# Performance work log

Hardware: AMD Instinct MI355X
Metric: run time of the kernel (lower is better)

Reference implementation:

```python
import jax, jax.numpy as jnp
import numpy as np

N = 50000      # num nodes
E = 800000     # num edges
F = 128        # num_node_features
H = 4          # num_heads
D = 32         # output_dim (per head); H*D == F -> residual is identity
G = 8          # grid_size
K = 3          # spline order (standard KANLinear default)
NEG_SLOPE = 0.2


def _make_grid(grid_size, k):
    # uniform grid on [-1, 1], extended by k on each side: [G + 2k + 1] points
    h = 2.0 / grid_size
    return jnp.arange(-k, grid_size + k + 1, dtype=jnp.float32) * h - 1.0


def _bsplines(x, grid, k):
    # x: [N, F], grid: [G+2k+1] -> bases: [N, F, G+k] (Cox-de Boor recursion)
    xg = x[..., None]
    b = ((xg >= grid[:-1]) & (xg < grid[1:])).astype(x.dtype)
    for j in range(1, k + 1):
        left = (xg - grid[:-(j + 1)]) / (grid[j:-1] - grid[:-(j + 1)]) * b[..., :-1]
        right = (grid[j + 1:] - xg) / (grid[j + 1:] - grid[1:-j]) * b[..., 1:]
        b = left + right
    return b


def _kan_linear(x, base_w, spline_w, grid, k):
    # efficient-KAN linear, no bias: silu(x) @ Wb^T + Bspline(x) contracted with Ws
    base = jax.nn.silu(x) @ base_w.T                      # [N, O]
    bs = _bsplines(x, grid, k)                            # [N, F, G+K]
    spline = jnp.einsum('nfc,ofc->no', bs, spline_w)      # [N, O]
    return base + spline


def setup_inputs() -> dict:
    key = jax.random.key(0)
    ks = jax.random.split(key, 8)
    O = H * D
    C = G + K
    x = jax.random.normal(ks[0], (N, F), dtype=jnp.float32)
    edge_index = jax.random.randint(ks[1], (2, E), 0, N, dtype=jnp.int64)
    scale = 1.0 / np.sqrt(F)
    base_w_src = jax.random.normal(ks[2], (O, F), dtype=jnp.float32) * scale
    spline_w_src = jax.random.normal(ks[3], (O, F, C), dtype=jnp.float32) * (0.1 * scale)
    base_w_dst = jax.random.normal(ks[4], (O, F), dtype=jnp.float32) * scale
    spline_w_dst = jax.random.normal(ks[5], (O, F, C), dtype=jnp.float32) * (0.1 * scale)
    double_attn = jax.random.normal(ks[6], (1, H, D), dtype=jnp.float32) * (1.0 / np.sqrt(D))
    bias = jnp.zeros((O,), dtype=jnp.float32)
    prelu_a = jnp.asarray(0.25, dtype=jnp.float32)  # nn.PReLU default
    return {"x": x, "edge_index": edge_index,
            "base_w_src": base_w_src, "spline_w_src": spline_w_src,
            "base_w_dst": base_w_dst, "spline_w_dst": spline_w_dst,
            "double_attn": double_attn, "bias": bias, "prelu_a": prelu_a}


def reference(x, edge_index, base_w_src, spline_w_src, base_w_dst, spline_w_dst,
              double_attn, bias, prelu_a):
    grid = _make_grid(G, K)
    src = edge_index[0]
    dst = edge_index[1]
    num_nodes = x.shape[0]
    # projections (dropout is identity in eval mode)
    sp = _kan_linear(x, base_w_src, spline_w_src, grid, K).reshape(num_nodes, H, D)
    dp = _kan_linear(x, base_w_dst, spline_w_dst, grid, K).reshape(num_nodes, H, D)
    # GATv2 edge scores: leakyrelu(gather(src) + gather(dst)), then attn vector dot
    e = jax.nn.leaky_relu(sp[src] + dp[dst], NEG_SLOPE)          # [E, H, D]
    attn = jnp.sum(double_attn * e, axis=-1)                     # [E, H]
    # segment softmax over incoming edges per destination node (global max shift, as in torch)
    exp_attn = jnp.exp(attn - jnp.max(attn))                     # [E, H]
    denom = jax.ops.segment_sum(exp_attn, dst, num_segments=num_nodes)  # [Nn, H]
    alpha = exp_attn / (denom[dst] + 1e-16)                      # [E, H]
    # weighted aggregation
    msg = sp[src] * alpha[..., None]                             # [E, H, D]
    out = jax.ops.segment_sum(msg, dst, num_segments=num_nodes)  # [Nn, H, D]
    # residual: num_node_features == H*D -> identity
    out = out + x.reshape(num_nodes, H, D)
    # concat heads + bias + PReLU activation
    out = out.reshape(num_nodes, H * D) + bias
    return jnp.where(out >= 0, out, prelu_a * out)
```

## Files before the change

kernel.cpp:

```cpp
#include <hip/hip_runtime.h>
#include <math.h>

#define NN 50000
#define EE 800000
#define FF 128
#define CC 11
#define O2 256
#define KT 1536
#define NKC 8
#define AROW 200
#define NPB 768
#define NTB2 224
#define NFB 1563
#define NPACK 424
#define NTN 896
#define CAP 64

typedef __attribute__((ext_vector_type(8))) short short8;
typedef __attribute__((ext_vector_type(4))) float f32x4;
typedef unsigned int uint;
typedef unsigned short ushort;

__device__ __forceinline__ ushort bf16_rne(float v) {
  uint u = __float_as_uint(v);
  u = u + 0x7FFFu + ((u >> 16) & 1u);
  return (ushort)(u >> 16);
}
__device__ __forceinline__ float bf_lo(uint u) { return __uint_as_float(u << 16); }
__device__ __forceinline__ float bf_hi(uint u) { return __uint_as_float(u & 0xffff0000u); }

__device__ __forceinline__ void lds_barrier() {
  asm volatile("s_waitcnt lgkmcnt(0)" ::: "memory");
  __builtin_amdgcn_s_barrier();
}

__global__ __launch_bounds__(256) void repack_zero_kernel(
    const float* __restrict__ bws, const float* __restrict__ sws,
    const float* __restrict__ bwd, const float* __restrict__ swd,
    ushort* __restrict__ Wh, int* __restrict__ cur) {
  int idx = blockIdx.x * 256 + threadIdx.x;
  if (idx < NN) cur[idx] = 0;
  if (idx >= O2 * KT) return;
  int j = idx & 7;
  int lane = (idx >> 3) & 63;
  int cg = (idx >> 9) & 15;
  int g = idx >> 13;
  int col = cg * 16 + (lane & 15);
  int k = g * 32 + (lane >> 4) * 8 + j;
  int f = k / 12;
  int ch = k - f * 12;
  const float* bw = (col < 128) ? bws : bwd;
  const float* sw = (col < 128) ? sws : swd;
  int o = col & 127;
  float v = (ch == 11) ? bw[(size_t)o * FF + f] : sw[((size_t)o * FF + f) * CC + ch];
  Wh[idx] = bf16_rne(v);
}

__device__ __forceinline__ void kan_row(float xv, ushort* row) {
  row[11] = bf16_rne(xv / (1.f + __expf(-xv)));
  float u = fmaf(xv, 4.f, 7.f);
  float fj = floorf(u);
  int j = (int)fj;
  if (j >= 0 && j <= 13) {
    float tt = u - fj;
    float t2 = tt * tt, t3 = t2 * tt;
    float w0 = (1.f / 6.f) * (1.f - 3.f * tt + 3.f * t2 - t3);
    float w1 = (1.f / 6.f) * (4.f - 6.f * t2 + 3.f * t3);
    float w2 = (1.f / 6.f) * (1.f + 3.f * tt + 3.f * t2 - 3.f * t3);
    float w3 = (1.f / 6.f) * t3;
    float wv[4] = {w0, w1, w2, w3};
    int i0 = j - 3;
#pragma unroll
    for (int c = 0; c < 4; ++c) {
      int idx = i0 + c;
      if (idx >= 0 && idx <= 10) row[idx] = bf16_rne(wv[c]);
    }
  }
}

__global__ __launch_bounds__(256) void proj_tail_kernel(
    const float* __restrict__ x, const ushort* __restrict__ Wh,
    uint* __restrict__ projB, float2* __restrict__ projF) {
  __shared__ ushort Ah[2][64][AROW];
  const int t = threadIdx.x;
  const int lane = t & 63;
  const int w = t >> 6;
  const int m = lane & 15;
  const int quad = lane >> 4;

  if (blockIdx.x >= NPB) {
    ushort(*Ath)[AROW] = Ah[0];
    const int tb = blockIdx.x - NPB;
    const int ks = tb & 7;
    const int rest = tb >> 3;
    const int tg = rest >> 1;
    const int hh = rest & 1;
    const int block0 = NPB * 64 + tg * 64;
    const int gn = block0 + lane;
    const bool valid = (gn < NN);

    {
      const float4 zero4 = make_float4(0.f, 0.f, 0.f, 0.f);
      float4 xvv = valid ? *(const float4*)(x + (size_t)gn * FF + ks * 16 + w * 4) : zero4;
      float xa[4] = {xvv.x, xvv.y, xvv.z, xvv.w};
      uint4* dz = (uint4*)&Ath[lane][w * 48];
#pragma unroll
      for (int i = 0; i < 6; ++i) dz[i] = make_uint4(0u, 0u, 0u, 0u);
#pragma unroll
      for (int jf = 0; jf < 4; ++jf) kan_row(xa[jf], &Ath[lane][w * 48 + jf * 12]);
    }

    f32x4 acc[4][2];
#pragma unroll
    for (int r = 0; r < 4; ++r)
#pragma unroll
      for (int c = 0; c < 2; ++c) acc[r][c] = (f32x4)(0.f);

    short8 bh_c[2];
#pragma unroll
    for (int c = 0; c < 2; ++c)
      bh_c[c] = *(const short8*)(Wh + (size_t)((ks * 6) * 16 + hh * 8 + w * 2 + c) * 512 +
                                 (size_t)lane * 8);
    __syncthreads();

#pragma unroll
    for (int sk = 0; sk < 6; ++sk) {
      short8 bh_n[2];
      if (sk < 5) {
#pragma unroll
        for (int c = 0; c < 2; ++c)
          bh_n[c] = *(const short8*)(Wh +
                                     (size_t)((ks * 6 + sk + 1) * 16 + hh * 8 + w * 2 + c) * 512 +
                                     (size_t)lane * 8);
      }
      short8 a0 = *(const short8*)(&Ath[0 * 16 + m][sk * 32 + quad * 8]);
      short8 a1 = *(const short8*)(&Ath[1 * 16 + m][sk * 32 + quad * 8]);
      short8 a2 = *(const short8*)(&Ath[2 * 16 + m][sk * 32 + quad * 8]);
      short8 a3 = *(const short8*)(&Ath[3 * 16 + m][sk * 32 + quad * 8]);
#pragma unroll
      for (int c = 0; c < 2; ++c) {
        acc[0][c] = __builtin_amdgcn_mfma_f32_16x16x32_bf16(a0, bh_c[c], acc[0][c], 0, 0, 0);
        acc[1][c] = __builtin_amdgcn_mfma_f32_16x16x32_bf16(a1, bh_c[c], acc[1][c], 0, 0, 0);
        acc[2][c] = __builtin_amdgcn_mfma_f32_16x16x32_bf16(a2, bh_c[c], acc[2][c], 0, 0, 0);
        acc[3][c] = __builtin_amdgcn_mfma_f32_16x16x32_bf16(a3, bh_c[c], acc[3][c], 0, 0, 0);
      }
      bh_c[0] = bh_n[0];
      bh_c[1] = bh_n[1];
    }
    const int q = hh * 4 + w;
#pragma unroll
    for (int r = 0; r < 4; ++r) {
#pragma unroll
      for (int reg = 0; reg < 4; ++reg) {
        int nl = r * 16 + quad * 4 + reg;
        projF[(size_t)(ks * NTN + tg * 64 + nl) * 128 + q * 16 + m] =
            make_float2(acc[r][0][reg], acc[r][1][reg]);
      }
    }
    return;
  }

  const int block0 = blockIdx.x * 64;
  const int gn = block0 + lane;

  auto stage = [&](float4 xvv, ushort(*buf)[AROW]) {
    float xa[4] = {xvv.x, xvv.y, xvv.z, xvv.w};
    uint4* dz = (uint4*)&buf[lane][w * 48];
#pragma unroll
    for (int i = 0; i < 6; ++i) dz[i] = make_uint4(0u, 0u, 0u, 0u);
#pragma unroll
    for (int jf = 0; jf < 4; ++jf) kan_row(xa[jf], &buf[lane][w * 48 + jf * 12]);
  };

  f32x4 acc[4][4];
#pragma unroll
  for (int r = 0; r < 4; ++r)
#pragma unroll
    for (int c = 0; c < 4; ++c) acc[r][c] = (f32x4)(0.f);

  float4 xv0 = *(const float4*)(x + (size_t)gn * FF + w * 4);
  stage(xv0, Ah[0]);
  float4 xv_next = *(const float4*)(x + (size_t)gn * FF + 16 + w * 4);

  short8 bh[2][4];
#pragma unroll
  for (int c = 0; c < 4; ++c) {
    bh[0][c] = *(const short8*)(Wh + (size_t)(0 * 16 + w * 4 + c) * 512 + (size_t)lane * 8);
    bh[1][c] = *(const short8*)(Wh + (size_t)(1 * 16 + w * 4 + c) * 512 + (size_t)lane * 8);
  }
  lds_barrier();

#pragma unroll 2
  for (int kc = 0; kc < NKC; ++kc) {
    float4 xv_pf = make_float4(0.f, 0.f, 0.f, 0.f);
    if (kc + 2 < NKC)
      xv_pf = *(const float4*)(x + (size_t)gn * FF + (kc + 2) * 16 + w * 4);
    if (kc + 1 < NKC) stage(xv_next, Ah[(kc + 1) & 1]);
#pragma unroll
    for (int sk = 0; sk < 6; ++sk) {
      const int p = sk & 1;
      short8 a0 = *(const short8*)(&Ah[kc & 1][0 * 16 + m][sk * 32 + quad * 8]);
      short8 a1 = *(const short8*)(&Ah[kc & 1][1 * 16 + m][sk * 32 + quad * 8]);
#pragma unroll
      for (int c = 0; c < 4; ++c)
        acc[0][c] = __builtin_amdgcn_mfma_f32_16x16x32_bf16(a0, bh[p][c], acc[0][c], 0, 0, 0);
#pragma unroll
      for (int c = 0; c < 4; ++c)
        acc[1][c] = __builtin_amdgcn_mfma_f32_16x16x32_bf16(a1, bh[p][c], acc[1][c], 0, 0, 0);
      short8 a2 = *(const short8*)(&Ah[kc & 1][2 * 16 + m][sk * 32 + quad * 8]);
      short8 a3 = *(const short8*)(&Ah[kc & 1][3 * 16 + m][sk * 32 + quad * 8]);
#pragma unroll
      for (int c = 0; c < 4; ++c)
        acc[2][c] = __builtin_amdgcn_mfma_f32_16x16x32_bf16(a2, bh[p][c], acc[2][c], 0, 0, 0);
#pragma unroll
      for (int c = 0; c < 4; ++c)
        acc[3][c] = __builtin_amdgcn_mfma_f32_16x16x32_bf16(a3, bh[p][c], acc[3][c], 0, 0, 0);
      int gnc = kc * 6 + sk + 2;
      if (gnc > 47) gnc = 47;
#pragma unroll
      for (int c = 0; c < 4; ++c)
        bh[p][c] = *(const short8*)(Wh + (size_t)(gnc * 16 + w * 4 + c) * 512 +
                                    (size_t)lane * 8);
    }
    lds_barrier();
    xv_next = xv_pf;
  }
#pragma unroll
  for (int r = 0; r < 4; ++r) {
#pragma unroll
    for (int reg = 0; reg < 4; ++reg) {
      int nd = block0 + r * 16 + quad * 4 + reg;
#pragma unroll
      for (int cp = 0; cp < 2; ++cp) {
        int q = 2 * w + cp;
        uint val = (uint)bf16_rne(acc[r][2 * cp][reg]) |
                   ((uint)bf16_rne(acc[r][2 * cp + 1][reg]) << 16);
        projB[(size_t)nd * 128 + q * 16 + m] = val;
      }
    }
  }
}

__global__ __launch_bounds__(256) void fill_kernel(
    const int* __restrict__ ei, int* __restrict__ cur, ushort* __restrict__ scsr) {
  int base = (blockIdx.x * 256 + threadIdx.x) * 2;
  if (base + 1 < EE) {
    int2 ss = *(const int2*)(ei + base);
    int2 dd = *(const int2*)(ei + EE + base);
    int p0 = atomicAdd(&cur[dd.x], 1);
    if (p0 < CAP) scsr[(size_t)dd.x * CAP + p0] = (ushort)ss.x;
    int p1 = atomicAdd(&cur[dd.y], 1);
    if (p1 < CAP) scsr[(size_t)dd.y * CAP + p1] = (ushort)ss.y;
  } else if (base < EE) {
    int s = ei[base], d = ei[EE + base];
    int p0 = atomicAdd(&cur[d], 1);
    if (p0 < CAP) scsr[(size_t)d * CAP + p0] = (ushort)s;
  }
}

__global__ __launch_bounds__(256) void pack_kernel(
    const float2* __restrict__ projF, uint* __restrict__ projB) {
  int wk = blockIdx.x * 256 + threadIdx.x;
  int n = wk >> 7, p = wk & 127;
  if (n < 848) {
    float lo = 0.f, hi = 0.f;
#pragma unroll
    for (int ks = 0; ks < 8; ++ks) {
      float2 v = projF[(size_t)(ks * NTN + n) * 128 + p];
      lo += v.x;
      hi += v.y;
    }
    projB[(size_t)(NPB * 64 + n) * 128 + p] =
        (uint)bf16_rne(lo) | ((uint)bf16_rne(hi) << 16);
  }
}

__global__ __launch_bounds__(256) void aggr_kernel(
    const uint* __restrict__ projB, const ushort* __restrict__ scsr,
    const int* __restrict__ cur, const float* __restrict__ av,
    const float* __restrict__ x, const float* __restrict__ bias,
    const float* __restrict__ pa, float* __restrict__ out) {
  int d = blockIdx.x * 4 + (threadIdx.x >> 6);
  if (d >= NN) return;
  int l = threadIdx.x & 63;
  int g = l >> 4, m = l & 15;
  const uint4* pb4 = (const uint4*)projB;
  int sv = (int)scsr[(size_t)d * CAP + l];
  uint4 dpu = pb4[(size_t)d * 32 + 16 + m];
  uint du[4] = {dpu.x, dpu.y, dpu.z, dpu.w};
  float dplo[4], dphi[4], avlo[4], avhi[4];
  int cl[4];
#pragma unroll
  for (int j = 0; j < 4; ++j) {
    dplo[j] = bf_lo(du[j]);
    dphi[j] = bf_hi(du[j]);
    int p = 4 * m + j;
    cl[j] = ((p >> 4) << 5) + (p & 15);
    avlo[j] = av[cl[j]];
    avhi[j] = av[cl[j] + 16];
  }
  int cnt = cur[d];
  if (cnt > CAP) cnt = CAP;
  float acl[4] = {0.f, 0.f, 0.f, 0.f}, ach[4] = {0.f, 0.f, 0.f, 0.f};
  float den = 0.f;
  if (cnt > 0 && g < cnt) {
    const int cm = cnt - 1;
    int e1 = g + 4, e2 = g + 8;
    int s0 = __shfl(sv, g, 64);
    int s1 = __shfl(sv, e1 < cm ? e1 : cm, 64);
    int s2 = __shfl(sv, e2 < cm ? e2 : cm, 64);
    uint4 U0 = pb4[(size_t)s0 * 32 + m];
    uint4 U1 = pb4[(size_t)s1 * 32 + m];
    uint4 U2 = pb4[(size_t)s2 * 32 + m];
    for (int e = g; e < cnt; e += 4) {
      int e3 = e + 12;
      int s3 = __shfl(sv, e3 < cm ? e3 : cm, 64);
      uint4 U3 = pb4[(size_t)s3 * 32 + m];
      uint uu[4] = {U0.x, U0.y, U0.z, U0.w};
      float slo[4], shi[4];
      float vp = 0.f;
#pragma unroll
      for (int j = 0; j < 4; ++j) {
        slo[j] = bf_lo(uu[j]);
        shi[j] = bf_hi(uu[j]);
        float v0 = slo[j] + dplo[j];
        float v1 = shi[j] + dphi[j];
        v0 = (v0 >= 0.f) ? v0 : 0.2f * v0;
        v1 = (v1 >= 0.f) ? v1 : 0.2f * v1;
        vp = fmaf(v0, avlo[j], vp);
        vp = fmaf(v1, avhi[j], vp);
      }
      vp += __shfl_xor(vp, 1, 64);
      vp += __shfl_xor(vp, 2, 64);
      float e_ = __expf(vp);
#pragma unroll
      for (int j = 0; j < 4; ++j) {
        acl[j] = fmaf(e_, slo[j], acl[j]);
        ach[j] = fmaf(e_, shi[j], ach[j]);
      }
      den += e_;
      U0 = U1;
      U1 = U2;
      U2 = U3;
    }
  }
#pragma unroll
  for (int off = 16; off < 64; off <<= 1) {
    den += __shfl_xor(den, off, 64);
#pragma unroll
    for (int j = 0; j < 4; ++j) {
      acl[j] += __shfl_xor(acl[j], off, 64);
      ach[j] += __shfl_xor(ach[j], off, 64);
    }
  }
  if (g == 0) {
    float a = pa[0];
    float r = 1.f / (den + 1e-16f);
#pragma unroll
    for (int j = 0; j < 4; ++j) {
      float o0 = acl[j] * r + x[(size_t)d * FF + cl[j]] + bias[cl[j]];
      float o1 = ach[j] * r + x[(size_t)d * FF + cl[j] + 16] + bias[cl[j] + 16];
      out[(size_t)d * FF + cl[j]] = (o0 >= 0.f) ? o0 : a * o0;
      out[(size_t)d * FF + cl[j] + 16] = (o1 >= 0.f) ? o1 : a * o1;
    }
  }
}

extern "C" void kernel_launch(void* const* d_in, const int* in_sizes, int n_in,
                              void* d_out, int out_size, void* d_ws, size_t ws_size,
                              hipStream_t stream) {
  const float* x = (const float*)d_in[0];
  const int* ei = (const int*)d_in[1];
  const float* bws = (const float*)d_in[2];
  const float* sws = (const float*)d_in[3];
  const float* bwd = (const float*)d_in[4];
  const float* swd = (const float*)d_in[5];
  const float* av = (const float*)d_in[6];
  const float* bias = (const float*)d_in[7];
  const float* pa = (const float*)d_in[8];

  ushort* Wh = (ushort*)d_ws;
  uint* projB = (uint*)(Wh + (size_t)O2 * KT);
  int* cur = (int*)(projB + (size_t)NN * 128);
  ushort* scsr = (ushort*)(cur + NN);
  float2* projF = (float2*)(scsr + (size_t)NN * CAP);

  repack_zero_kernel<<<(O2 * KT + 255) / 256, 256, 0, stream>>>(bws, sws, bwd, swd, Wh, cur);
  proj_tail_kernel<<<NPB + NTB2, 256, 0, stream>>>(x, Wh, projB, projF);
  fill_kernel<<<NFB, 256, 0, stream>>>(ei, cur, scsr);
  pack_kernel<<<NPACK, 256, 0, stream>>>(projF, projB);
  aggr_kernel<<<(NN + 3) / 4, 256, 0, stream>>>(projB, scsr, cur, av, x, bias, pa,
                                                (float*)d_out);
}
```

Measured before the change: 221.4 us.

## Privatize CSR fill counters per XCC to avoid cross-die atomic contention

The fill kernel now reads the hardware XCC id and writes each edge into one of eight per-XCC bucket arrays, each with its own counter and a capacity of 24 per destination. This keeps the atomics and scattered stores local to one die instead of contending across dies. The aggregation kernel reads all eight counters, computes prefix offsets, and gathers each lane's source index from the matching bucket. In exchange it zeroes an eight times larger counter array, adds eight counter loads per destination, and truncates edges if one XCC gets more than 24 edges for a node.

```diff
diff --git a/kernel.cpp b/kernel.cpp
--- a/kernel.cpp
+++ b/kernel.cpp
@@ -15,6 +15,7 @@
 #define NPACK 424
 #define NTN 896
 #define CAP 64
+#define CAP8 24
 
 typedef __attribute__((ext_vector_type(8))) short short8;
 typedef __attribute__((ext_vector_type(4))) float f32x4;
@@ -37,9 +38,11 @@
 __global__ __launch_bounds__(256) void repack_zero_kernel(
     const float* __restrict__ bws, const float* __restrict__ sws,
     const float* __restrict__ bwd, const float* __restrict__ swd,
-    ushort* __restrict__ Wh, int* __restrict__ cur) {
+    ushort* __restrict__ Wh, int* __restrict__ cur8) {
   int idx = blockIdx.x * 256 + threadIdx.x;
-  if (idx < NN) cur[idx] = 0;
+  if (idx < 8 * NN) cur8[idx] = 0;
+  int idx2 = idx + 393216;
+  if (idx2 < 8 * NN) cur8[idx2] = 0;
   if (idx >= O2 * KT) return;
   int j = idx & 7;
   int lane = (idx >> 3) & 63;
@@ -242,19 +245,25 @@
 }
 
 __global__ __launch_bounds__(256) void fill_kernel(
-    const int* __restrict__ ei, int* __restrict__ cur, ushort* __restrict__ scsr) {
+    const int* __restrict__ ei, int* __restrict__ cur8, ushort* __restrict__ scsr8) {
+  uint xcc;
+  asm volatile("s_getreg_b32 %0, hwreg(HW_REG_XCC_ID)" : "=s"(xcc));
+  xcc &= 7;
   int base = (blockIdx.x * 256 + threadIdx.x) * 2;
   if (base + 1 < EE) {
     int2 ss = *(const int2*)(ei + base);
     int2 dd = *(const int2*)(ei + EE + base);
-    int p0 = atomicAdd(&cur[dd.x], 1);
-    if (p0 < CAP) scsr[(size_t)dd.x * CAP + p0] = (ushort)ss.x;
-    int p1 = atomicAdd(&cur[dd.y], 1);
-    if (p1 < CAP) scsr[(size_t)dd.y * CAP + p1] = (ushort)ss.y;
+    size_t b0 = (size_t)xcc * NN + dd.x;
+    int p0 = atomicAdd(&cur8[b0], 1);
+    if (p0 < CAP8) scsr8[b0 * CAP8 + p0] = (ushort)ss.x;
+    size_t b1 = (size_t)xcc * NN + dd.y;
+    int p1 = atomicAdd(&cur8[b1], 1);
+    if (p1 < CAP8) scsr8[b1 * CAP8 + p1] = (ushort)ss.y;
   } else if (base < EE) {
     int s = ei[base], d = ei[EE + base];
-    int p0 = atomicAdd(&cur[d], 1);
-    if (p0 < CAP) scsr[(size_t)d * CAP + p0] = (ushort)s;
+    size_t b0 = (size_t)xcc * NN + d;
+    int p0 = atomicAdd(&cur8[b0], 1);
+    if (p0 < CAP8) scsr8[b0 * CAP8 + p0] = (ushort)s;
   }
 }
 
@@ -276,8 +285,8 @@
 }
 
 __global__ __launch_bounds__(256) void aggr_kernel(
-    const uint* __restrict__ projB, const ushort* __restrict__ scsr,
-    const int* __restrict__ cur, const float* __restrict__ av,
+    const uint* __restrict__ projB, const ushort* __restrict__ scsr8,
+    const int* __restrict__ cur8, const float* __restrict__ av,
     const float* __restrict__ x, const float* __restrict__ bias,
     const float* __restrict__ pa, float* __restrict__ out) {
   int d = blockIdx.x * 4 + (threadIdx.x >> 6);
@@ -285,7 +294,23 @@
   int l = threadIdx.x & 63;
   int g = l >> 4, m = l & 15;
   const uint4* pb4 = (const uint4*)projB;
-  int sv = (int)scsr[(size_t)d * CAP + l];
+  int c8[8];
+#pragma unroll
+  for (int s = 0; s < 8; ++s) {
+    int cs = cur8[(size_t)s * NN + d];
+    c8[s] = (cs > CAP8) ? CAP8 : cs;
+  }
+  int acc0 = 0, mys = -1, myi = 0;
+#pragma unroll
+  for (int s = 0; s < 8; ++s) {
+    if (mys < 0 && l < acc0 + c8[s]) { mys = s; myi = l - acc0; }
+    acc0 += c8[s];
+  }
+  int cnt = (acc0 > CAP) ? CAP : acc0;
+  int sv = 0;
+  if (mys >= 0 && l < CAP)
+    sv = (int)scsr8[((size_t)mys * NN + d) * CAP8 + myi];
+
   uint4 dpu = pb4[(size_t)d * 32 + 16 + m];
   uint du[4] = {dpu.x, dpu.y, dpu.z, dpu.w};
   float dplo[4], dphi[4], avlo[4], avhi[4];
@@ -299,8 +324,6 @@
     avlo[j] = av[cl[j]];
     avhi[j] = av[cl[j] + 16];
   }
-  int cnt = cur[d];
-  if (cnt > CAP) cnt = CAP;
   float acl[4] = {0.f, 0.f, 0.f, 0.f}, ach[4] = {0.f, 0.f, 0.f, 0.f};
   float den = 0.f;
   if (cnt > 0 && g < cnt) {
@@ -381,14 +404,14 @@
 
   ushort* Wh = (ushort*)d_ws;
   uint* projB = (uint*)(Wh + (size_t)O2 * KT);
-  int* cur = (int*)(projB + (size_t)NN * 128);
-  ushort* scsr = (ushort*)(cur + NN);
-  float2* projF = (float2*)(scsr + (size_t)NN * CAP);
-
-  repack_zero_kernel<<<(O2 * KT + 255) / 256, 256, 0, stream>>>(bws, sws, bwd, swd, Wh, cur);
+  int* cur8 = (int*)(projB + (size_t)NN * 128);
+  ushort* scsr8 = (ushort*)(cur8 + 8 * NN);
+  float2* projF = (float2*)(scsr8 + (size_t)8 * NN * CAP8);
+
+  repack_zero_kernel<<<(O2 * KT + 255) / 256, 256, 0, stream>>>(bws, sws, bwd, swd, Wh, cur8);
   proj_tail_kernel<<<NPB + NTB2, 256, 0, stream>>>(x, Wh, projB, projF);
-  fill_kernel<<<NFB, 256, 0, stream>>>(ei, cur, scsr);
+  fill_kernel<<<NFB, 256, 0, stream>>>(ei, cur8, scsr8);
   pack_kernel<<<NPACK, 256, 0, stream>>>(projF, projB);
-  aggr_kernel<<<(NN + 3) / 4, 256, 0, stream>>>(projB, scsr, cur, av, x, bias, pa,
+  aggr_kernel<<<(NN + 3) / 4, 256, 0, stream>>>(projB, scsr8, cur8, av, x, bias, pa,
                                                 (float*)d_out);
 }
```

Measured after the change: 217.4 us. About the same (-1.8%).
